# Kernel optimization log

Measured on AMD Instinct MI355X. Metric: run time of the kernel, lower is better.

The kernel has to match this reference:

```python
import jax, jax.numpy as jnp
import numpy as np

MAX_PERIOD = 10000.0


def _rope(x, ts):
    # x: [B,H,T,D], ts: [B,T] integer positions (per-batch offset + arange(T))
    B, H, T, D = x.shape
    half = D // 2
    freqs = jnp.exp(jnp.arange(half, dtype=jnp.float32) * (-np.log(MAX_PERIOD) * 2.0 / D))
    ang = ts.astype(jnp.float32)[:, None, :, None] * freqs  # [B,1,T,half]
    cos, sin = jnp.cos(ang), jnp.sin(ang)
    xr = x.reshape(B, H, T, half, 2)  # interleaved (real, imag) pairs
    r, i = xr[..., 0], xr[..., 1]
    out = jnp.stack([r * cos - i * sin, r * sin + i * cos], axis=-1)
    return out.reshape(B, H, T, D)


def setup_inputs() -> dict:
    key = jax.random.key(0)
    ks = jax.random.split(key, 7)
    B, T, C = 8, 128, 1024
    H, D, CAP = 16, 64, 2048
    return {
        'x': jax.random.normal(ks[0], (B, T, C), dtype=jnp.float32),
        'w_in': jax.random.normal(ks[1], (3 * C, C), dtype=jnp.float32) * 0.02,
        'w_out': jax.random.normal(ks[2], (C, C), dtype=jnp.float32) * 0.02,
        'cache_k': jax.random.normal(ks[3], (B, H, CAP, D), dtype=jnp.float32),
        'cache_v': jax.random.normal(ks[4], (B, H, CAP, D), dtype=jnp.float32),
        'end_offset': jax.random.randint(ks[5], (B,), 0, CAP).astype(jnp.int64) if jax.config.jax_enable_x64 else jax.random.randint(ks[5], (B,), 0, CAP),
        'exec_mask': jnp.ones((B,), dtype=bool),
    }


def reference(x, w_in, w_out, cache_k, cache_v, end_offset, exec_mask):
    B, T, C = x.shape
    H, CAP = cache_k.shape[1], cache_k.shape[2]
    D = C // H
    context = CAP  # capacity == self.context

    # fused in-projection, split per rearrange 'b t (p h d) -> p b h t d', p=3
    qkv = (x @ w_in.T).reshape(B, T, 3, H, D).transpose(2, 0, 3, 1, 4)
    q, k, v = qkv[0], qkv[1], qkv[2]  # each [B,H,T,D]

    ts = end_offset[:, None] + jnp.arange(T)  # [B,T] absolute positions of new tokens
    q = _rope(q, ts)
    k = _rope(k, ts)

    # ring-buffer scatter (RingKVCache.complete)
    idx = ts % CAP  # [B,T]
    bI = jnp.arange(B)[:, None, None]
    hI = jnp.arange(H)[None, :, None]
    cache_k = cache_k.at[bI, hI, idx[:, None, :]].set(k)
    cache_v = cache_v.at[bI, hI, idx[:, None, :]].set(v)

    # absolute position of every cache slot, -1 for invalid slots
    cap_idx = jnp.arange(CAP)
    last = end_offset + T - 1  # [B]
    end_index = last % CAP
    delta = cap_idx[None, :] - end_index[:, None]  # [B,CAP]
    positions = jnp.where(delta <= 0, last[:, None] + delta, last[:, None] + delta - CAP)
    new_end = jnp.where(exec_mask, end_offset + T, end_offset)
    positions = jnp.where(cap_idx[None, :] >= new_end[:, None], -1, positions)

    # causal + context mask derived from positions
    d = ts[:, :, None] - positions[:, None, :]  # [B,T,CAP]
    mask = (positions[:, None, :] >= 0) & (d >= 0) & (d < context)

    scale = 1.0 / np.sqrt(D)
    scores = jnp.einsum('bhtd,bhsd->bhts', q, cache_k) * scale  # [B,H,T,CAP]
    scores = jnp.where(mask[:, None], scores, jnp.asarray(-1e9, scores.dtype))
    attn = jax.nn.softmax(scores, axis=-1)
    out = jnp.einsum('bhts,bhsd->bhtd', attn, cache_v)
    out = out.transpose(0, 2, 1, 3).reshape(B, T, C)  # 'b h t d -> b t (h d)'
    return out @ w_out.T
```

## Files before the change

### kernel.cpp

```cpp
#include <hip/hip_runtime.h>
#include <math.h>

#define BB 8
#define TT 128
#define CC 1024
#define HH 16
#define DD 64
#define CAP 2048
#define NSPLIT 4

typedef __attribute__((ext_vector_type(8))) short short8;
typedef __attribute__((ext_vector_type(4))) short short4v;
typedef __attribute__((ext_vector_type(4))) float float4v;
typedef _Float16 half8 __attribute__((ext_vector_type(8)));
typedef _Float16 half4v __attribute__((ext_vector_type(4)));

__device__ __forceinline__ short f2bf(float x) {
    union { float f; unsigned u; } un; un.f = x;
    unsigned r = (un.u + 0x7FFF + ((un.u >> 16) & 1)) >> 16;
    return (short)r;
}
__device__ __forceinline__ float bf2f(unsigned short h) {
    union { unsigned u; float f; } un; un.u = ((unsigned)h) << 16;
    return un.f;
}

__global__ __launch_bounds__(256) void split_all(const float* __restrict__ x,
                                                 const float* __restrict__ w_in,
                                                 const float* __restrict__ w_out,
                                                 _Float16* __restrict__ xhi,
                                                 _Float16* __restrict__ xlo,
                                                 _Float16* __restrict__ wh,
                                                 _Float16* __restrict__ woh) {
    size_t i = ((size_t)blockIdx.x * 256 + threadIdx.x) * 4;
    if (i < (size_t)1048576) {
        float4 f = *(const float4*)(x + i);
        half4v h, l;
        h.x = (_Float16)f.x; l.x = (_Float16)(f.x - (float)h.x);
        h.y = (_Float16)f.y; l.y = (_Float16)(f.y - (float)h.y);
        h.z = (_Float16)f.z; l.z = (_Float16)(f.z - (float)h.z);
        h.w = (_Float16)f.w; l.w = (_Float16)(f.w - (float)h.w);
        *(half4v*)(xhi + i) = h;
        *(half4v*)(xlo + i) = l;
    } else if (i < (size_t)4194304) {
        size_t off = i - 1048576;
        float4 f = *(const float4*)(w_in + off);
        half4v h;
        h.x = (_Float16)f.x; h.y = (_Float16)f.y; h.z = (_Float16)f.z; h.w = (_Float16)f.w;
        *(half4v*)(wh + off) = h;
    } else {
        size_t off = i - 4194304;
        float4 f = *(const float4*)(w_out + off);
        half4v h;
        h.x = (_Float16)f.x; h.y = (_Float16)f.y; h.z = (_Float16)f.z; h.w = (_Float16)f.w;
        *(half4v*)(woh + off) = h;
    }
}

template <int ROWS>
__device__ __forceinline__ void stage_glds(const unsigned short* __restrict__ src,
                                           unsigned short* lds, int K, int wv, int lane) {
#pragma unroll
    for (int c = wv; c < ROWS / 16; c += 4) {
        int row = c * 16 + (lane >> 2);
        int g = lane & 3;
        const unsigned short* ga = src + (size_t)row * K + g * 8;
        unsigned short* la = lds + c * 512 + lane * 8;
        __builtin_amdgcn_global_load_lds((__attribute__((address_space(1))) const unsigned short*)ga,
                                         (__attribute__((address_space(3))) unsigned short*)la,
                                         16, 0, 0);
    }
}

template <int MT, int NT>
__global__ __launch_bounds__(256) void gemm_f16x2(const _Float16* __restrict__ Ahi,
                                                  const _Float16* __restrict__ Alo,
                                                  const _Float16* __restrict__ Bh,
                                                  float* __restrict__ C, int M, int N, int K) {
    constexpr int BM = 2 * MT * 16, BN = 2 * NT * 16;
    __shared__ __align__(16) _Float16 As_h[BM * 32];
    __shared__ __align__(16) _Float16 As_l[BM * 32];
    __shared__ __align__(16) _Float16 Bs[BN * 32];

    int tid = threadIdx.x;
    int lane = tid & 63, wv = tid >> 6;
    int wr = wv >> 1, wc = wv & 1;
    int quad = lane >> 4, lq = lane & 15;
    int m0 = blockIdx.y * BM, n0 = blockIdx.x * BN;

    float4v acc[MT][NT];
#pragma unroll
    for (int mt = 0; mt < MT; ++mt)
#pragma unroll
        for (int nt = 0; nt < NT; ++nt) acc[mt][nt] = (float4v){0.f, 0.f, 0.f, 0.f};

    const unsigned short* a_h = (const unsigned short*)(Ahi + (size_t)m0 * K);
    const unsigned short* a_l = (const unsigned short*)(Alo + (size_t)m0 * K);
    const unsigned short* b_h = (const unsigned short*)(Bh + (size_t)n0 * K);

    for (int k0 = 0; k0 < K; k0 += 32) {
        __syncthreads();
        stage_glds<BM>(a_h + k0, (unsigned short*)As_h, K, wv, lane);
        stage_glds<BM>(a_l + k0, (unsigned short*)As_l, K, wv, lane);
        stage_glds<BN>(b_h + k0, (unsigned short*)Bs, K, wv, lane);
        __syncthreads();

        half8 ah[MT], al[MT];
#pragma unroll
        for (int mt = 0; mt < MT; ++mt) {
            int row = wr * MT * 16 + mt * 16 + lq;
            ah[mt] = *(const half8*)&As_h[row * 32 + quad * 8];
            al[mt] = *(const half8*)&As_l[row * 32 + quad * 8];
        }
#pragma unroll
        for (int nt = 0; nt < NT; ++nt) {
            int row = wc * NT * 16 + nt * 16 + lq;
            half8 bh = *(const half8*)&Bs[row * 32 + quad * 8];
#pragma unroll
            for (int mt = 0; mt < MT; ++mt) {
                float4v c = acc[mt][nt];
                c = __builtin_amdgcn_mfma_f32_16x16x32_f16(ah[mt], bh, c, 0, 0, 0);
                c = __builtin_amdgcn_mfma_f32_16x16x32_f16(al[mt], bh, c, 0, 0, 0);
                acc[mt][nt] = c;
            }
        }
    }

#pragma unroll
    for (int mt = 0; mt < MT; ++mt)
#pragma unroll
        for (int nt = 0; nt < NT; ++nt) {
            int n = n0 + wc * NT * 16 + nt * 16 + lq;
#pragma unroll
            for (int r = 0; r < 4; ++r) {
                int m = m0 + wr * MT * 16 + mt * 16 + quad * 4 + r;
                C[(size_t)m * N + n] = acc[mt][nt][r];
            }
        }
}

__global__ __launch_bounds__(256) void rope_scatter(const float* __restrict__ qkv,
                                                    unsigned short* __restrict__ q_bf,
                                                    float* __restrict__ cache_k,
                                                    float* __restrict__ cache_v,
                                                    const int* __restrict__ end_offset) {
    int gid = blockIdx.x * 256 + threadIdx.x;
    int j = gid & 31;
    int h = (gid >> 5) & 15;
    int t = (gid >> 9) & 127;
    int b = gid >> 16;

    int ts = end_offset[b] + t;
    int slot = ts & (CAP - 1);

    float freq = expf(-0.28782313662425574f * (float)j);
    float ang = (float)ts * freq;
    float s, c;
    sincosf(ang, &s, &c);

    const float* base = qkv + (size_t)(b * TT + t) * (3 * CC);
    int col = h * DD + 2 * j;
    float2 qv = *(const float2*)&base[col];
    float2 kv = *(const float2*)&base[CC + col];
    float2 vv = *(const float2*)&base[2 * CC + col];

    float qr = qv.x * c - qv.y * s;
    float qi = qv.x * s + qv.y * c;
    float kr = kv.x * c - kv.y * s;
    float ki = kv.x * s + kv.y * c;

    size_t qo = ((size_t)(b * HH + h) * TT + t) * DD + 2 * j;
    ushort2 qp;
    qp.x = (unsigned short)f2bf(qr);
    qp.y = (unsigned short)f2bf(qi);
    *(ushort2*)&q_bf[qo] = qp;
    size_t ko = ((size_t)(b * HH + h) * CAP + slot) * DD + 2 * j;
    *(float2*)&cache_k[ko] = make_float2(kr, ki);
    *(float2*)&cache_v[ko] = vv;
}

__global__ __launch_bounds__(256) void attn_mfma(const unsigned short* __restrict__ qb,
                                                 const float* __restrict__ ck,
                                                 const float* __restrict__ cv,
                                                 const int* __restrict__ endo,
                                                 const unsigned char* __restrict__ emb,
                                                 const int* __restrict__ emi,
                                                 float* __restrict__ pacc012,
                                                 float* __restrict__ pacc3,
                                                 float* __restrict__ pml) {
    __shared__ __align__(16) short k_s[64 * 72];
    __shared__ __align__(16) short v_t[64 * 64];
    __shared__ __align__(16) short p_s[4][16 * 72];
    __shared__ float stat_s[4][16];

    int tid = threadIdx.x;
    int lane = tid & 63, wv = tid >> 6;
    int quad = lane >> 4, lq = lane & 15;
    int hb = blockIdx.x;
    int h = hb & 15, b = hb >> 4;
    int qc2 = blockIdx.y;
    int sid = blockIdx.z;
    int qrow = qc2 * 64 + wv * 16 + lq;

    int end0 = endo[b];
    int em = (emb[b] != 0) || (emi[b] != 0);
    int last = end0 + TT - 1;
    int end_index = last & (CAP - 1);
    int new_end = em ? (end0 + TT) : end0;
    int se = new_end < CAP ? new_end : CAP;
    int ntiles = (se + 63) >> 6;
    int tps = (ntiles + NSPLIT - 1) / NSPLIT;
    int t0 = sid * tps;
    int t1 = t0 + tps < ntiles ? t0 + tps : ntiles;

    const unsigned short* qrp = qb + ((size_t)(b * HH + h) * TT + qrow) * DD;
    short8 aq0 = *(const short8*)(qrp + quad * 8);
    short8 aq1 = *(const short8*)(qrp + 32 + quad * 8);

    const float* kg = ck + (size_t)(b * HH + h) * CAP * DD;
    const float* vg = cv + (size_t)(b * HH + h) * CAP * DD;

    int k_row = tid >> 4, k_f4 = tid & 15;
    float4 kreg[4];
    float vreg[2][8];

    float m[4], l[4];
#pragma unroll
    for (int r = 0; r < 4; ++r) { m[r] = 0.0f; l[r] = 0.f; }
    float4v acc[4];
#pragma unroll
    for (int mt = 0; mt < 4; ++mt) acc[mt] = (float4v){0.f, 0.f, 0.f, 0.f};

    if (t0 < t1) {
        int sb = t0 * 64;
#pragma unroll
        for (int i = 0; i < 4; ++i)
            kreg[i] = *(const float4*)&kg[(size_t)(sb + k_row + 16 * i) * DD + k_f4 * 4];
#pragma unroll
        for (int gi = 0; gi < 2; ++gi) {
            int g = wv + gi * 4;
#pragma unroll
            for (int i = 0; i < 8; ++i)
                vreg[gi][i] = vg[(size_t)(sb + g * 8 + i) * DD + lane];
        }
    }

    for (int t = t0; t < t1; ++t) {
        int s0 = t * 64;
        __syncthreads();
#pragma unroll
        for (int i = 0; i < 4; ++i) {
            float4 f = kreg[i];
            short4v sv;
            sv.x = f2bf(f.x); sv.y = f2bf(f.y); sv.z = f2bf(f.z); sv.w = f2bf(f.w);
            *(short4v*)&k_s[(k_row + 16 * i) * 72 + k_f4 * 4] = sv;
        }
#pragma unroll
        for (int gi = 0; gi < 2; ++gi) {
            int g = wv + gi * 4;
            short8 pk;
#pragma unroll
            for (int i = 0; i < 8; ++i) pk[i] = f2bf(vreg[gi][i]);
            *(short8*)&v_t[lane * 64 + (g ^ (lane & 7)) * 8] = pk;
        }
        __syncthreads();
        if (t + 1 < t1) {
            int sn = s0 + 64;
#pragma unroll
            for (int i = 0; i < 4; ++i)
                kreg[i] = *(const float4*)&kg[(size_t)(sn + k_row + 16 * i) * DD + k_f4 * 4];
#pragma unroll
            for (int gi = 0; gi < 2; ++gi) {
                int g = wv + gi * 4;
#pragma unroll
                for (int i = 0; i < 8; ++i)
                    vreg[gi][i] = vg[(size_t)(sn + g * 8 + i) * DD + lane];
            }
        }

        float4v sc[4];
#pragma unroll
        for (int nt = 0; nt < 4; ++nt) {
            const short* kr = &k_s[(nt * 16 + lq) * 72 + quad * 8];
            short8 bk0 = *(const short8*)kr;
            short8 bk1 = *(const short8*)(kr + 32);
            float4v c = (float4v){0.f, 0.f, 0.f, 0.f};
            c = __builtin_amdgcn_mfma_f32_16x16x32_bf16(aq0, bk0, c, 0, 0, 0);
            c = __builtin_amdgcn_mfma_f32_16x16x32_bf16(aq1, bk1, c, 0, 0, 0);
            sc[nt] = c;
        }

        float x[4][4];
#pragma unroll
        for (int nt = 0; nt < 4; ++nt) {
            int s = s0 + nt * 16 + lq;
            int delta = s - end_index;
            int pos = (delta <= 0) ? (last + delta) : (last + delta - CAP);
            if (s >= new_end) pos = -1;
#pragma unroll
            for (int r = 0; r < 4; ++r) {
                int tq = end0 + qc2 * 64 + wv * 16 + quad * 4 + r;
                int dd = tq - pos;
                bool valid = (pos >= 0) && (dd >= 0) && (dd < CAP);
                x[nt][r] = valid ? sc[nt][r] * 0.125f : -1.0e30f;
            }
        }
        float al[4];
#pragma unroll
        for (int r = 0; r < 4; ++r) {
            float vm = fmaxf(fmaxf(x[0][r], x[1][r]), fmaxf(x[2][r], x[3][r]));
            vm = fmaxf(vm, __shfl_xor(vm, 1, 64));
            vm = fmaxf(vm, __shfl_xor(vm, 2, 64));
            vm = fmaxf(vm, __shfl_xor(vm, 4, 64));
            vm = fmaxf(vm, __shfl_xor(vm, 8, 64));
            float mn = fmaxf(m[r], vm);
            al[r] = __expf(m[r] - mn);
            float ps = 0.f;
#pragma unroll
            for (int nt = 0; nt < 4; ++nt) {
                float p = __expf(x[nt][r] - mn);
                x[nt][r] = p;
                ps += p;
            }
            ps += __shfl_xor(ps, 1, 64);
            ps += __shfl_xor(ps, 2, 64);
            ps += __shfl_xor(ps, 4, 64);
            ps += __shfl_xor(ps, 8, 64);
            l[r] = l[r] * al[r] + ps;
            m[r] = mn;
        }
#pragma unroll
        for (int r = 0; r < 4; ++r)
#pragma unroll
            for (int nt = 0; nt < 4; ++nt)
                p_s[wv][(quad * 4 + r) * 72 + nt * 16 + lq] = f2bf(x[nt][r]);
        if (lq == 0) {
#pragma unroll
            for (int r = 0; r < 4; ++r) stat_s[wv][quad * 4 + r] = al[r];
        }

        float af = stat_s[wv][lq];
        short8 bp0 = *(const short8*)&p_s[wv][lq * 72 + quad * 8];
        short8 bp1 = *(const short8*)&p_s[wv][lq * 72 + 32 + quad * 8];
#pragma unroll
        for (int mt = 0; mt < 4; ++mt) {
            int d = mt * 16 + lq;
            const short* vr = &v_t[d * 64];
            short8 av0 = *(const short8*)(vr + ((quad ^ (d & 7)) * 8));
            short8 av1 = *(const short8*)(vr + (((4 + quad) ^ (d & 7)) * 8));
            float4v a = acc[mt];
            a.x *= af; a.y *= af; a.z *= af; a.w *= af;
            a = __builtin_amdgcn_mfma_f32_16x16x32_bf16(av0, bp0, a, 0, 0, 0);
            a = __builtin_amdgcn_mfma_f32_16x16x32_bf16(av1, bp1, a, 0, 0, 0);
            acc[mt] = a;
        }
    }

    int base_row = (b * HH + h) * TT + qc2 * 64;
    float* pa = (sid < 3) ? (pacc012 + (size_t)sid * (16384 * 64)) : pacc3;
    int row_g = base_row + wv * 16 + lq;
#pragma unroll
    for (int mt = 0; mt < 4; ++mt)
        *(float4v*)&pa[(size_t)row_g * 64 + mt * 16 + quad * 4] = acc[mt];
    if (lq == 0) {
#pragma unroll
        for (int r = 0; r < 4; ++r) {
            int rg = base_row + wv * 16 + quad * 4 + r;
            size_t ix = ((size_t)sid * 16384 + rg) * 2;
            pml[ix] = m[r];
            pml[ix + 1] = l[r];
        }
    }
}

__global__ __launch_bounds__(256) void attn_combine(const float* __restrict__ pacc012,
                                                    const float* __restrict__ pacc3,
                                                    const float* __restrict__ pml,
                                                    _Float16* __restrict__ ahi,
                                                    _Float16* __restrict__ alo) {
    int gid = blockIdx.x * 256 + threadIdx.x;
    int row = gid >> 6, d = gid & 63;

    float mv[NSPLIT], lv[NSPLIT];
#pragma unroll
    for (int s = 0; s < NSPLIT; ++s) {
        size_t ix = ((size_t)s * 16384 + row) * 2;
        mv[s] = pml[ix];
        lv[s] = pml[ix + 1];
    }
    float M = fmaxf(fmaxf(mv[0], mv[1]), fmaxf(mv[2], mv[3]));
    float O = 0.f, L = 0.f;
#pragma unroll
    for (int s = 0; s < NSPLIT; ++s) {
        const float* pa = (s < 3) ? (pacc012 + (size_t)s * (16384 * 64)) : pacc3;
        float w = __expf(mv[s] - M);
        L += w * lv[s];
        O += w * pa[(size_t)row * 64 + d];
    }
    float o = (L > 0.f) ? (O / L) : 0.f;

    int b = row >> 11, h = (row >> 7) & 15, q = row & 127;
    size_t ob = ((size_t)(b * TT + q)) * CC + h * DD + d;
    _Float16 hi = (_Float16)o;
    ahi[ob] = hi;
    alo[ob] = (_Float16)(o - (float)hi);
}

extern "C" void kernel_launch(void* const* d_in, const int* in_sizes, int n_in,
                              void* d_out, int out_size, void* d_ws, size_t ws_size,
                              hipStream_t stream) {
    const float* x = (const float*)d_in[0];
    const float* w_in = (const float*)d_in[1];
    const float* w_out = (const float*)d_in[2];
    float* cache_k = (float*)d_in[3];
    float* cache_v = (float*)d_in[4];
    const int* end_offset = (const int*)d_in[5];
    const unsigned char* exec_mask_b = (const unsigned char*)d_in[6];
    const int* exec_mask_i = (const int*)d_in[6];
    float* out = (float*)d_out;

    float* qkv = (float*)d_ws;
    unsigned short* q_bf = (unsigned short*)(qkv + (size_t)1024 * 3072);
    _Float16* xhi = (_Float16*)(q_bf + (size_t)1024 * 1024);
    _Float16* xlo = xhi + (size_t)1024 * 1024;
    _Float16* wh = xlo + (size_t)1024 * 1024;
    _Float16* woh = wh + (size_t)3072 * 1024;
    _Float16* ahi = woh + (size_t)1024 * 1024;
    _Float16* alo = ahi + (size_t)1024 * 1024;

    float* pacc012 = qkv;
    float* pacc3 = (float*)xhi;
    float* pml = (float*)wh;

    split_all<<<5120, 256, 0, stream>>>(x, w_in, w_out, xhi, xlo, wh, woh);
    gemm_f16x2<2, 4><<<dim3(3072 / 128, 1024 / 64), 256, 0, stream>>>(
        xhi, xlo, wh, qkv, BB * TT, 3 * CC, CC);
    rope_scatter<<<(BB * TT * HH * 32) / 256, 256, 0, stream>>>(qkv, q_bf, cache_k, cache_v, end_offset);
    attn_mfma<<<dim3(HH * BB, 2, NSPLIT), 256, 0, stream>>>(q_bf, cache_k, cache_v, end_offset,
                                                            exec_mask_b, exec_mask_i,
                                                            pacc012, pacc3, pml);
    attn_combine<<<(16384 * 64) / 256, 256, 0, stream>>>(pacc012, pacc3, pml, ahi, alo);
    gemm_f16x2<2, 2><<<dim3(1024 / 64, 1024 / 64), 256, 0, stream>>>(
        ahi, alo, woh, out, BB * TT, CC, CC);
}
```

Before: 239.0 us.

## Rework attention softmax layout, interleave KV splits, fold scale, retile GEMMs

The attention kernel swaps the MFMA operand order so each lane owns one query row. That removes the per-row shuffle reductions and the LDS round trip for the alpha stats. KV tiles are now interleaved across splits (stride NSPLIT) for load balance, block indices are remapped, and a fast path skips mask arithmetic for fully valid tiles. Other changes: the 1/sqrt(D) scale is folded into q during rope, bf16 packing uses the hardware v_cvt_pk_bf16_f32 instruction, and both projection GEMMs get smaller tile configurations for more blocks. The simplified mask drops some conditions and relies on input structure, so it risks subtle correctness differences.

```diff
diff --git a/kernel.cpp b/kernel.cpp
--- a/kernel.cpp
+++ b/kernel.cpp
@@ -20,9 +20,10 @@
     unsigned r = (un.u + 0x7FFF + ((un.u >> 16) & 1)) >> 16;
     return (short)r;
 }
-__device__ __forceinline__ float bf2f(unsigned short h) {
-    union { unsigned u; float f; } un; un.u = ((unsigned)h) << 16;
-    return un.f;
+__device__ __forceinline__ unsigned cvt_pk_bf16(float a, float b) {
+    unsigned r;
+    asm("v_cvt_pk_bf16_f32 %0, %1, %2" : "=v"(r) : "v"(a), "v"(b));
+    return r;
 }
 
 __global__ __launch_bounds__(256) void split_all(const float* __restrict__ x,
@@ -171,8 +172,8 @@
 
     size_t qo = ((size_t)(b * HH + h) * TT + t) * DD + 2 * j;
     ushort2 qp;
-    qp.x = (unsigned short)f2bf(qr);
-    qp.y = (unsigned short)f2bf(qi);
+    qp.x = (unsigned short)f2bf(qr * 0.125f);
+    qp.y = (unsigned short)f2bf(qi * 0.125f);
     *(ushort2*)&q_bf[qo] = qp;
     size_t ko = ((size_t)(b * HH + h) * CAP + slot) * DD + 2 * j;
     *(float2*)&cache_k[ko] = make_float2(kr, ki);
@@ -191,15 +192,15 @@
     __shared__ __align__(16) short k_s[64 * 72];
     __shared__ __align__(16) short v_t[64 * 64];
     __shared__ __align__(16) short p_s[4][16 * 72];
-    __shared__ float stat_s[4][16];
 
     int tid = threadIdx.x;
     int lane = tid & 63, wv = tid >> 6;
     int quad = lane >> 4, lq = lane & 15;
-    int hb = blockIdx.x;
+    int f = blockIdx.x + 128 * (blockIdx.y + 2 * blockIdx.z);
+    int sid = f & 3;
+    int qc2 = (f >> 2) & 1;
+    int hb = f >> 3;
     int h = hb & 15, b = hb >> 4;
-    int qc2 = blockIdx.y;
-    int sid = blockIdx.z;
     int qrow = qc2 * 64 + wv * 16 + lq;
 
     int end0 = endo[b];
@@ -209,9 +210,11 @@
     int new_end = em ? (end0 + TT) : end0;
     int se = new_end < CAP ? new_end : CAP;
     int ntiles = (se + 63) >> 6;
-    int tps = (ntiles + NSPLIT - 1) / NSPLIT;
-    int t0 = sid * tps;
-    int t1 = t0 + tps < ntiles ? t0 + tps : ntiles;
+
+    int tq = end0 + qrow;
+    int tq0 = end0 + qc2 * 64 + wv * 16;
+    int len_bad = last - tq0;
+    int a_bad = (tq0 + 1) & (CAP - 1);
 
     const unsigned short* qrp = qb + ((size_t)(b * HH + h) * TT + qrow) * DD;
     short8 aq0 = *(const short8*)(qrp + quad * 8);
@@ -224,15 +227,13 @@
     float4 kreg[4];
     float vreg[2][8];
 
-    float m[4], l[4];
-#pragma unroll
-    for (int r = 0; r < 4; ++r) { m[r] = 0.0f; l[r] = 0.f; }
+    float m = 0.f, l = 0.f;
     float4v acc[4];
 #pragma unroll
     for (int mt = 0; mt < 4; ++mt) acc[mt] = (float4v){0.f, 0.f, 0.f, 0.f};
 
-    if (t0 < t1) {
-        int sb = t0 * 64;
+    if (sid < ntiles) {
+        int sb = sid * 64;
 #pragma unroll
         for (int i = 0; i < 4; ++i)
             kreg[i] = *(const float4*)&kg[(size_t)(sb + k_row + 16 * i) * DD + k_f4 * 4];
@@ -245,27 +246,31 @@
         }
     }
 
-    for (int t = t0; t < t1; ++t) {
+    for (int t = sid; t < ntiles; t += NSPLIT) {
         int s0 = t * 64;
         __syncthreads();
 #pragma unroll
         for (int i = 0; i < 4; ++i) {
-            float4 f = kreg[i];
-            short4v sv;
-            sv.x = f2bf(f.x); sv.y = f2bf(f.y); sv.z = f2bf(f.z); sv.w = f2bf(f.w);
-            *(short4v*)&k_s[(k_row + 16 * i) * 72 + k_f4 * 4] = sv;
+            float4 fv = kreg[i];
+            uint2 u;
+            u.x = cvt_pk_bf16(fv.x, fv.y);
+            u.y = cvt_pk_bf16(fv.z, fv.w);
+            *(uint2*)&k_s[(k_row + 16 * i) * 72 + k_f4 * 4] = u;
         }
 #pragma unroll
         for (int gi = 0; gi < 2; ++gi) {
             int g = wv + gi * 4;
-            short8 pk;
-#pragma unroll
-            for (int i = 0; i < 8; ++i) pk[i] = f2bf(vreg[gi][i]);
-            *(short8*)&v_t[lane * 64 + (g ^ (lane & 7)) * 8] = pk;
+            uint4 u;
+            u.x = cvt_pk_bf16(vreg[gi][0], vreg[gi][1]);
+            u.y = cvt_pk_bf16(vreg[gi][2], vreg[gi][3]);
+            u.z = cvt_pk_bf16(vreg[gi][4], vreg[gi][5]);
+            u.w = cvt_pk_bf16(vreg[gi][6], vreg[gi][7]);
+            *(uint4*)&v_t[lane * 64 + (g ^ (lane & 7)) * 8] = u;
         }
         __syncthreads();
-        if (t + 1 < t1) {
-            int sn = s0 + 64;
+        int tn = t + NSPLIT;
+        if (tn < ntiles) {
+            int sn = tn * 64;
 #pragma unroll
             for (int i = 0; i < 4; ++i)
                 kreg[i] = *(const float4*)&kg[(size_t)(sn + k_row + 16 * i) * DD + k_f4 * 4];
@@ -285,61 +290,63 @@
             short8 bk0 = *(const short8*)kr;
             short8 bk1 = *(const short8*)(kr + 32);
             float4v c = (float4v){0.f, 0.f, 0.f, 0.f};
-            c = __builtin_amdgcn_mfma_f32_16x16x32_bf16(aq0, bk0, c, 0, 0, 0);
-            c = __builtin_amdgcn_mfma_f32_16x16x32_bf16(aq1, bk1, c, 0, 0, 0);
+            c = __builtin_amdgcn_mfma_f32_16x16x32_bf16(bk0, aq0, c, 0, 0, 0);
+            c = __builtin_amdgcn_mfma_f32_16x16x32_bf16(bk1, aq1, c, 0, 0, 0);
             sc[nt] = c;
         }
 
+        int off = (s0 - a_bad) & (CAP - 1);
+        bool fast = (off >= len_bad) && (off <= CAP - 64) && (s0 + 63 < se);
         float x[4][4];
-#pragma unroll
-        for (int nt = 0; nt < 4; ++nt) {
-            int s = s0 + nt * 16 + lq;
-            int delta = s - end_index;
-            int pos = (delta <= 0) ? (last + delta) : (last + delta - CAP);
-            if (s >= new_end) pos = -1;
+        if (fast) {
+#pragma unroll
+            for (int nt = 0; nt < 4; ++nt)
+#pragma unroll
+                for (int r = 0; r < 4; ++r) x[nt][r] = sc[nt][r];
+        } else {
+#pragma unroll
+            for (int nt = 0; nt < 4; ++nt)
+#pragma unroll
+                for (int r = 0; r < 4; ++r) {
+                    int s = s0 + nt * 16 + quad * 4 + r;
+                    int delta = s - end_index;
+                    int pos = (delta <= 0) ? (last + delta) : (last + delta - CAP);
+                    bool valid = (s < se) && (pos <= tq);
+                    x[nt][r] = valid ? sc[nt][r] : -1.0e30f;
+                }
+        }
+
+        float v01 = fmaxf(fmaxf(x[0][0], x[0][1]), fmaxf(x[0][2], x[0][3]));
+        float v23 = fmaxf(fmaxf(x[1][0], x[1][1]), fmaxf(x[1][2], x[1][3]));
+        float v45 = fmaxf(fmaxf(x[2][0], x[2][1]), fmaxf(x[2][2], x[2][3]));
+        float v67 = fmaxf(fmaxf(x[3][0], x[3][1]), fmaxf(x[3][2], x[3][3]));
+        float vm = fmaxf(fmaxf(v01, v23), fmaxf(v45, v67));
+        vm = fmaxf(vm, __shfl_xor(vm, 16, 64));
+        vm = fmaxf(vm, __shfl_xor(vm, 32, 64));
+        float mn = fmaxf(m, vm);
+        float al = __expf(m - mn);
+        float ps = 0.f;
+#pragma unroll
+        for (int nt = 0; nt < 4; ++nt)
 #pragma unroll
             for (int r = 0; r < 4; ++r) {
-                int tq = end0 + qc2 * 64 + wv * 16 + quad * 4 + r;
-                int dd = tq - pos;
-                bool valid = (pos >= 0) && (dd >= 0) && (dd < CAP);
-                x[nt][r] = valid ? sc[nt][r] * 0.125f : -1.0e30f;
-            }
-        }
-        float al[4];
-#pragma unroll
-        for (int r = 0; r < 4; ++r) {
-            float vm = fmaxf(fmaxf(x[0][r], x[1][r]), fmaxf(x[2][r], x[3][r]));
-            vm = fmaxf(vm, __shfl_xor(vm, 1, 64));
-            vm = fmaxf(vm, __shfl_xor(vm, 2, 64));
-            vm = fmaxf(vm, __shfl_xor(vm, 4, 64));
-            vm = fmaxf(vm, __shfl_xor(vm, 8, 64));
-            float mn = fmaxf(m[r], vm);
-            al[r] = __expf(m[r] - mn);
-            float ps = 0.f;
-#pragma unroll
-            for (int nt = 0; nt < 4; ++nt) {
                 float p = __expf(x[nt][r] - mn);
                 x[nt][r] = p;
                 ps += p;
             }
-            ps += __shfl_xor(ps, 1, 64);
-            ps += __shfl_xor(ps, 2, 64);
-            ps += __shfl_xor(ps, 4, 64);
-            ps += __shfl_xor(ps, 8, 64);
-            l[r] = l[r] * al[r] + ps;
-            m[r] = mn;
-        }
-#pragma unroll
-        for (int r = 0; r < 4; ++r)
-#pragma unroll
-            for (int nt = 0; nt < 4; ++nt)
-                p_s[wv][(quad * 4 + r) * 72 + nt * 16 + lq] = f2bf(x[nt][r]);
-        if (lq == 0) {
-#pragma unroll
-            for (int r = 0; r < 4; ++r) stat_s[wv][quad * 4 + r] = al[r];
-        }
-
-        float af = stat_s[wv][lq];
+        ps += __shfl_xor(ps, 16, 64);
+        ps += __shfl_xor(ps, 32, 64);
+        l = l * al + ps;
+        m = mn;
+
+#pragma unroll
+        for (int nt = 0; nt < 4; ++nt) {
+            uint2 u;
+            u.x = cvt_pk_bf16(x[nt][0], x[nt][1]);
+            u.y = cvt_pk_bf16(x[nt][2], x[nt][3]);
+            *(uint2*)&p_s[wv][lq * 72 + nt * 16 + quad * 4] = u;
+        }
+
         short8 bp0 = *(const short8*)&p_s[wv][lq * 72 + quad * 8];
         short8 bp1 = *(const short8*)&p_s[wv][lq * 72 + 32 + quad * 8];
 #pragma unroll
@@ -349,7 +356,7 @@
             short8 av0 = *(const short8*)(vr + ((quad ^ (d & 7)) * 8));
             short8 av1 = *(const short8*)(vr + (((4 + quad) ^ (d & 7)) * 8));
             float4v a = acc[mt];
-            a.x *= af; a.y *= af; a.z *= af; a.w *= af;
+            a.x *= al; a.y *= al; a.z *= al; a.w *= al;
             a = __builtin_amdgcn_mfma_f32_16x16x32_bf16(av0, bp0, a, 0, 0, 0);
             a = __builtin_amdgcn_mfma_f32_16x16x32_bf16(av1, bp1, a, 0, 0, 0);
             acc[mt] = a;
@@ -362,14 +369,10 @@
 #pragma unroll
     for (int mt = 0; mt < 4; ++mt)
         *(float4v*)&pa[(size_t)row_g * 64 + mt * 16 + quad * 4] = acc[mt];
-    if (lq == 0) {
-#pragma unroll
-        for (int r = 0; r < 4; ++r) {
-            int rg = base_row + wv * 16 + quad * 4 + r;
-            size_t ix = ((size_t)sid * 16384 + rg) * 2;
-            pml[ix] = m[r];
-            pml[ix + 1] = l[r];
-        }
+    if (quad == 0) {
+        size_t ix = ((size_t)sid * 16384 + row_g) * 2;
+        pml[ix] = m;
+        pml[ix + 1] = l;
     }
 }
 
@@ -433,13 +436,13 @@
     float* pml = (float*)wh;
 
     split_all<<<5120, 256, 0, stream>>>(x, w_in, w_out, xhi, xlo, wh, woh);
-    gemm_f16x2<2, 4><<<dim3(3072 / 128, 1024 / 64), 256, 0, stream>>>(
+    gemm_f16x2<2, 2><<<dim3(3072 / 64, 1024 / 64), 256, 0, stream>>>(
         xhi, xlo, wh, qkv, BB * TT, 3 * CC, CC);
     rope_scatter<<<(BB * TT * HH * 32) / 256, 256, 0, stream>>>(qkv, q_bf, cache_k, cache_v, end_offset);
     attn_mfma<<<dim3(HH * BB, 2, NSPLIT), 256, 0, stream>>>(q_bf, cache_k, cache_v, end_offset,
                                                             exec_mask_b, exec_mask_i,
                                                             pacc012, pacc3, pml);
     attn_combine<<<(16384 * 64) / 256, 256, 0, stream>>>(pacc012, pacc3, pml, ahi, alo);
-    gemm_f16x2<2, 2><<<dim3(1024 / 64, 1024 / 64), 256, 0, stream>>>(
+    gemm_f16x2<1, 2><<<dim3(1024 / 64, 1024 / 32), 256, 0, stream>>>(
         ahi, alo, woh, out, BB * TT, CC, CC);
 }
```

Result: faster. 223.7 us (-6.4%).
